# Optimization experiments

Measured on AMD Instinct MI355X. Metric: run time of the kernel, lower is better.

The kernel has to match this reference:

```python
import jax, jax.numpy as jnp
import numpy as np

N_NODES = 16384
N_EDGES = 98304
N_CAND = 1024
# GAT config from default __init__: heads=[8,8,1], features=[3,64,128,64]
LAYERS = [
    (3, 8, 64, True, True),      # (f_in, n_heads, f_out, concat, elu)
    (512, 8, 128, True, True),
    (1024, 1, 64, False, False),
]


def _gat_layer(x, src, tgt, W, a_src, a_tgt, b, skipW, nh, fo, concat, act):
    n = x.shape[0]
    proj = (x @ W).reshape(n, nh, fo)                 # [N, NH, F]
    s_src = jnp.einsum('nhf,hf->nh', proj, a_src)     # [N, NH]
    s_tgt = jnp.einsum('nhf,hf->nh', proj, a_tgt)
    e = jax.nn.leaky_relu(s_src[src] + s_tgt[tgt], 0.2)   # [E, NH]
    # numerically stable segment softmax over incoming edges of each target node
    e_max = jax.ops.segment_max(e, tgt, num_segments=n)
    ex = jnp.exp(e - jax.lax.stop_gradient(e_max)[tgt])
    denom = jax.ops.segment_sum(ex, tgt, num_segments=n)
    alpha = ex / (denom[tgt] + 1e-16)                 # [E, NH]
    agg = jax.ops.segment_sum(proj[src] * alpha[:, :, None], tgt, num_segments=n)
    out = agg + (x @ skipW).reshape(n, nh, fo)        # skip connection (projected)
    out = out.reshape(n, nh * fo) if concat else out.mean(axis=1)
    out = out + b
    return jax.nn.elu(out) if act else out


def setup_inputs() -> dict:
    key = jax.random.key(0)
    ks = iter(jax.random.split(key, 32))
    d = {}
    d['fea'] = jax.random.normal(next(ks), (N_NODES, 3), dtype=jnp.float32)
    d['edge_index'] = jax.random.randint(next(ks), (2, N_EDGES), 0, N_NODES, dtype=jnp.int32)
    d['candidates_id'] = jax.random.randint(next(ks), (N_CAND,), 0, N_NODES, dtype=jnp.int32)
    for i, (fi, nh, fo, concat, _) in enumerate(LAYERS):
        sc = 1.0 / np.sqrt(fi)
        d[f'W{i}'] = jax.random.normal(next(ks), (fi, nh * fo), dtype=jnp.float32) * sc
        d[f'a_src{i}'] = jax.random.normal(next(ks), (nh, fo), dtype=jnp.float32) * 0.1
        d[f'a_tgt{i}'] = jax.random.normal(next(ks), (nh, fo), dtype=jnp.float32) * 0.1
        d[f'b{i}'] = jnp.zeros((nh * fo if concat else fo,), dtype=jnp.float32)
        d[f'skip{i}'] = jax.random.normal(next(ks), (fi, nh * fo), dtype=jnp.float32) * sc
    # MLP head build_mlp(256, 3, 64, 1): 64->256 Tanh 256->256 Tanh 256->1
    for j, (a, bdim) in enumerate([(64, 256), (256, 256), (256, 1)], start=1):
        d[f'mW{j}'] = jax.random.normal(next(ks), (a, bdim), dtype=jnp.float32) / np.sqrt(a)
        d[f'mb{j}'] = jnp.zeros((bdim,), dtype=jnp.float32)
    return d


def reference(fea, edge_index, candidates_id,
              W0, a_src0, a_tgt0, b0, skip0,
              W1, a_src1, a_tgt1, b1, skip1,
              W2, a_src2, a_tgt2, b2, skip2,
              mW1, mb1, mW2, mb2, mW3, mb3):
    src, tgt = edge_index[0], edge_index[1]
    x = fea
    params = [(W0, a_src0, a_tgt0, b0, skip0), (W1, a_src1, a_tgt1, b1, skip1),
              (W2, a_src2, a_tgt2, b2, skip2)]
    for (fi, nh, fo, concat, act), (W, asr, atg, b, sk) in zip(LAYERS, params):
        x = _gat_layer(x, src, tgt, W, asr, atg, b, sk, nh, fo, concat, act)
    cand = x[candidates_id]                              # [C, 64]
    h = jnp.tanh(cand @ mW1 + mb1)
    h = jnp.tanh(h @ mW2 + mb2)
    prob = (h @ mW3 + mb3).squeeze(-1)                   # [C]
    return prob, candidates_id
```

## Files before the change

### kernel.cpp

```cpp
#include <hip/hip_runtime.h>
#include <cmath>

#define N_NODES 16384
#define N_EDGES 98304
#define N_CAND  1024

typedef __bf16 bf16x8 __attribute__((ext_vector_type(8)));
typedef short  s16x8  __attribute__((ext_vector_type(8)));
typedef float  f32x4  __attribute__((ext_vector_type(4)));
typedef unsigned short u16x2 __attribute__((ext_vector_type(2)));
typedef unsigned short u16x4 __attribute__((ext_vector_type(4)));

__device__ __forceinline__ unsigned short f2bf(float x) {
    unsigned u = __float_as_uint(x);
    return (unsigned short)((u + 0x7fffu + ((u >> 16) & 1u)) >> 16);
}
__device__ __forceinline__ float bf2f(unsigned short b) {
    return __uint_as_float((unsigned)b << 16);
}

#define GLL(gp, lp) __builtin_amdgcn_global_load_lds(                          \
    (const __attribute__((address_space(1))) unsigned int*)(const void*)(gp),  \
    (__attribute__((address_space(3))) unsigned int*)(void*)(lp), 16, 0, 0)

__global__ __launch_bounds__(256) void k_hist(const int* __restrict__ tgt,
                                              int* __restrict__ deg) {
    int e = blockIdx.x * 256 + threadIdx.x;
    if (e < N_EDGES) atomicAdd(&deg[tgt[e]], 1);
}

__global__ __launch_bounds__(256) void k_scan_all(const int* __restrict__ deg,
                                                  int* __restrict__ off,
                                                  int* __restrict__ cursor) {
    __shared__ int ts[256];
    int tid = threadIdx.x;
    const int4* d4 = (const int4*)(deg + tid * 64);
    int s = 0;
    #pragma unroll
    for (int i = 0; i < 16; ++i) {
        int4 v = d4[i];
        s += v.x + v.y + v.z + v.w;
    }
    ts[tid] = s;
    __syncthreads();
    for (int o = 1; o < 256; o <<= 1) {
        int t = (tid >= o) ? ts[tid - o] : 0;
        __syncthreads();
        ts[tid] += t;
        __syncthreads();
    }
    int run = ts[tid] - s;
    int4* o4 = (int4*)(off + tid * 64);
    int4* c4 = (int4*)(cursor + tid * 64);
    #pragma unroll
    for (int i = 0; i < 16; ++i) {
        int4 v = d4[i];
        int4 ov;
        ov.x = run; run += v.x;
        ov.y = run; run += v.y;
        ov.z = run; run += v.z;
        ov.w = run; run += v.w;
        o4[i] = ov;
        c4[i] = ov;
    }
    if (tid == 255) off[N_NODES] = run;
}

__global__ __launch_bounds__(256) void k_scatter(const int* __restrict__ ei,
                                                 int* __restrict__ cursor,
                                                 int* __restrict__ csrc) {
    int e = blockIdx.x * 256 + threadIdx.x;
    if (e < N_EDGES) {
        int s = ei[e];
        int t = ei[N_EDGES + e];
        int pos = atomicAdd(&cursor[t], 1);
        csrc[pos] = s;
    }
}

__global__ __launch_bounds__(256) void k_l0s(const float* __restrict__ fea,
                                             const float* __restrict__ W0,
                                             const float* __restrict__ as,
                                             const float* __restrict__ at,
                                             float* __restrict__ ssrc,
                                             float* __restrict__ stgt) {
    int n = blockIdx.x, tid = threadIdx.x;
    float f0 = fea[n * 3 + 0], f1 = fea[n * 3 + 1], f2 = fea[n * 3 + 2];
    int c1 = tid, c2 = tid + 256;
    float p1 = f0 * W0[c1] + f1 * W0[512 + c1] + f2 * W0[1024 + c1];
    float p2 = f0 * W0[c2] + f1 * W0[512 + c2] + f2 * W0[1024 + c2];
    float vs1 = p1 * as[c1], vt1 = p1 * at[c1];
    float vs2 = p2 * as[c2], vt2 = p2 * at[c2];
    #pragma unroll
    for (int o = 32; o; o >>= 1) {
        vs1 += __shfl_xor(vs1, o); vt1 += __shfl_xor(vt1, o);
        vs2 += __shfl_xor(vs2, o); vt2 += __shfl_xor(vt2, o);
    }
    int lane = tid & 63, w = tid >> 6;
    if (lane == 0) {
        ssrc[n * 8 + w]     = vs1;  stgt[n * 8 + w]     = vt1;
        ssrc[n * 8 + w + 4] = vs2;  stgt[n * 8 + w + 4] = vt2;
    }
}

__device__ __forceinline__ void pack_slot(const float* __restrict__ src0,
                                          const float* __restrict__ src1,
                                          int splitN, int NTOT, int NKB, int s,
                                          unsigned short* __restrict__ hi,
                                          unsigned short* __restrict__ lo) {
    int nb = s / (NKB * 512);
    int rem = s - nb * (NKB * 512);
    int kb = rem >> 9;
    int sl = rem & 511;
    int c = sl >> 7, n = sl & 127;
    int col = nb * 128 + n;
    const float* src;
    int cc, stride;
    if (col < splitN) { src = src0; cc = col; stride = splitN; }
    else              { src = src1; cc = col - splitN; stride = NTOT - splitN; }
    int k0 = kb * 32 + c * 8;
    s16x8 hv, lv;
    #pragma unroll
    for (int j = 0; j < 8; ++j) {
        float w = src[(size_t)(k0 + j) * stride + cc];
        unsigned short h = f2bf(w);
        hv[j] = (short)h;
        lv[j] = (short)f2bf(w - bf2f(h));
    }
    *(s16x8*)(hi + (size_t)s * 8) = hv;
    *(s16x8*)(lo + (size_t)s * 8) = lv;
}

__global__ __launch_bounds__(256) void k_pack_all(
    const float* __restrict__ W1, const float* __restrict__ sk1,
    unsigned short* __restrict__ pw1h, unsigned short* __restrict__ pw1l,
    const float* __restrict__ W2, const float* __restrict__ sk2,
    unsigned short* __restrict__ pw2h, unsigned short* __restrict__ pw2l) {
    int s = blockIdx.x * 256 + threadIdx.x;
    if (s < 131072) {
        pack_slot(W1, sk1, 1024, 2048, 16, s, pw1h, pw1l);
    } else {
        int s2 = s - 131072;
        if (s2 < 16384) pack_slot(W2, sk2, 64, 128, 32, s2, pw2h, pw2l);
    }
}

template <int F, int NTOT, int KS>
__global__ __launch_bounds__(256, 2) void k_gemm_mfma(
    const unsigned short* __restrict__ Xhi, const unsigned short* __restrict__ Xlo,
    const unsigned short* __restrict__ Wph, const unsigned short* __restrict__ Wpl,
    float* __restrict__ out0, float* __restrict__ out1, int splitN) {
    constexpr int NKB = F / 32;
    static_assert(KS == 1 || NTOT == 128, "split-K assumes single col-block");
    __shared__ unsigned short lds[2 * 16384];
    const int tid = threadIdx.x;
    const int bm  = blockIdx.y * 128;
    const int nb  = blockIdx.x;

    const int sA0 = tid, sA1 = tid + 256;
    const int rA0 = sA0 >> 2, rA1 = sA1 >> 2;
    const int cA0 = (sA0 & 3) ^ ((rA0 >> 1) & 3);
    const int cA1 = (sA1 & 3) ^ ((rA1 >> 1) & 3);
    const unsigned short* gAh0 = Xhi + (size_t)(bm + rA0) * F + cA0 * 8;
    const unsigned short* gAh1 = Xhi + (size_t)(bm + rA1) * F + cA1 * 8;
    const unsigned short* gAl0 = Xlo + (size_t)(bm + rA0) * F + cA0 * 8;
    const unsigned short* gAl1 = Xlo + (size_t)(bm + rA1) * F + cA1 * 8;
    const unsigned short* gBh  = Wph + (KS == 1 ? (size_t)nb * NKB * 4096 : 0);
    const unsigned short* gBl  = Wpl + (KS == 1 ? (size_t)nb * NKB * 4096 : 0);

    const int wave = tid >> 6, lane = tid & 63;
    const int wm = wave >> 1, wn = wave & 1;
    const int l15 = lane & 15, lc = lane >> 4;

    int offA[4], offB[4];
    #pragma unroll
    for (int mi = 0; mi < 4; ++mi) {
        int row = wm * 64 + mi * 16 + l15;
        int chp = lc ^ ((row >> 1) & 3);
        offA[mi] = row * 32 + chp * 8;
    }
    #pragma unroll
    for (int ni = 0; ni < 4; ++ni) {
        int n = wn * 64 + ni * 16 + l15;
        offB[ni] = 8192 + (lc * 128 + n) * 8;
    }

    f32x4 acc[4][4];
    #pragma unroll
    for (int i = 0; i < 4; ++i)
        #pragma unroll
        for (int j = 0; j < 4; ++j)
            acc[i][j] = (f32x4){0.f, 0.f, 0.f, 0.f};

    auto stage = [&](int kb, int buf) {
        unsigned short* l = &lds[buf * 16384];
        const size_t ka  = (size_t)kb * 32;
        const size_t kbb = (size_t)kb * 4096;
        GLL(gAh0 + ka, l + sA0 * 8);
        GLL(gAh1 + ka, l + sA1 * 8);
        GLL(gAl0 + ka, l + 4096 + sA0 * 8);
        GLL(gAl1 + ka, l + 4096 + sA1 * 8);
        GLL(gBh + kbb + sA0 * 8, l + 8192 + sA0 * 8);
        GLL(gBh + kbb + sA1 * 8, l + 8192 + sA1 * 8);
        GLL(gBl + kbb + sA0 * 8, l + 12288 + sA0 * 8);
        GLL(gBl + kbb + sA1 * 8, l + 12288 + sA1 * 8);
    };

    const int kb0 = (KS > 1) ? nb * (NKB / KS) : 0;
    const int kbN = (KS > 1) ? (NKB / KS) : NKB;

    stage(kb0, 0);
    __syncthreads();

    for (int ki = 0; ki < kbN; ++ki) {
        const int buf = ki & 1;
        if (ki + 1 < kbN) stage(kb0 + ki + 1, buf ^ 1);
        const unsigned short* l = &lds[buf * 16384];
        bf16x8 ah[4], al[4], bh[4], bl[4];
        #pragma unroll
        for (int mi = 0; mi < 4; ++mi) {
            ah[mi] = *(const bf16x8*)(l + offA[mi]);
            al[mi] = *(const bf16x8*)(l + 4096 + offA[mi]);
        }
        #pragma unroll
        for (int ni = 0; ni < 4; ++ni) {
            bh[ni] = *(const bf16x8*)(l + offB[ni]);
            bl[ni] = *(const bf16x8*)(l + 4096 + offB[ni]);
        }
        #pragma unroll
        for (int mi = 0; mi < 4; ++mi)
            #pragma unroll
            for (int ni = 0; ni < 4; ++ni) {
                acc[mi][ni] = __builtin_amdgcn_mfma_f32_16x16x32_bf16(ah[mi], bh[ni], acc[mi][ni], 0, 0, 0);
                acc[mi][ni] = __builtin_amdgcn_mfma_f32_16x16x32_bf16(ah[mi], bl[ni], acc[mi][ni], 0, 0, 0);
                acc[mi][ni] = __builtin_amdgcn_mfma_f32_16x16x32_bf16(al[mi], bh[ni], acc[mi][ni], 0, 0, 0);
            }
        __syncthreads();
    }

    if constexpr (KS > 1) {
        #pragma unroll
        for (int ni = 0; ni < 4; ++ni) {
            int col = wn * 64 + ni * 16 + l15;
            #pragma unroll
            for (int mi = 0; mi < 4; ++mi) {
                int row0 = bm + wm * 64 + mi * 16 + lc * 4;
                #pragma unroll
                for (int r = 0; r < 4; ++r)
                    out0[((size_t)nb * N_NODES + row0 + r) * NTOT + col] = acc[mi][ni][r];
            }
        }
    } else {
        #pragma unroll
        for (int ni = 0; ni < 4; ++ni) {
            int col = nb * 128 + wn * 64 + ni * 16 + l15;
            float* o;
            int cc, stride;
            if (col < splitN) { o = out0; cc = col; stride = splitN; }
            else              { o = out1; cc = col - splitN; stride = NTOT - splitN; }
            #pragma unroll
            for (int mi = 0; mi < 4; ++mi) {
                int row0 = bm + wm * 64 + mi * 16 + lc * 4;
                #pragma unroll
                for (int r = 0; r < 4; ++r)
                    o[(size_t)(row0 + r) * stride + cc] = acc[mi][ni][r];
            }
        }
    }
}

template <int H, int FO>
__global__ __launch_bounds__(256) void k_scores(const float* __restrict__ P,
                                                const float* __restrict__ asrc,
                                                const float* __restrict__ atgt,
                                                float* __restrict__ ssrc,
                                                float* __restrict__ stgt) {
    constexpr int K = H * FO;
    int gid  = blockIdx.x * 4 + (threadIdx.x >> 6);
    int lane = threadIdx.x & 63;
    int n = gid / H, h = gid - n * H;
    if (n >= N_NODES) return;
    float vs = 0.f, vt = 0.f;
    #pragma unroll
    for (int q = 0; q < FO / 64; ++q) {
        int f = lane + q * 64;
        float p = P[(size_t)n * K + h * FO + f];
        vs += p * asrc[h * FO + f];
        vt += p * atgt[h * FO + f];
    }
    #pragma unroll
    for (int o = 32; o; o >>= 1) {
        vs += __shfl_xor(vs, o);
        vt += __shfl_xor(vt, o);
    }
    if (lane == 0) {
        ssrc[n * H + h] = vs;
        stgt[n * H + h] = vt;
    }
}

__global__ __launch_bounds__(256) void k_red2s(const float* __restrict__ part,
                                               const float* __restrict__ as2,
                                               const float* __restrict__ at2,
                                               float* __restrict__ P2,
                                               float* __restrict__ S2,
                                               float* __restrict__ ssrc,
                                               float* __restrict__ stgt) {
    int tid = threadIdx.x;
    int node = blockIdx.x * 16 + (tid >> 4);
    int cg = tid & 15;
    int c0 = cg * 8;
    const float* p0 = part + (size_t)node * 128 + c0;
    float v[8];
    {
        float4 a = *(const float4*)(p0);
        float4 b = *(const float4*)(p0 + 4);
        v[0]=a.x; v[1]=a.y; v[2]=a.z; v[3]=a.w; v[4]=b.x; v[5]=b.y; v[6]=b.z; v[7]=b.w;
    }
    #pragma unroll
    for (int ks = 1; ks < 4; ++ks) {
        const float* pk = p0 + (size_t)ks * N_NODES * 128;
        float4 a = *(const float4*)(pk);
        float4 b = *(const float4*)(pk + 4);
        v[0]+=a.x; v[1]+=a.y; v[2]+=a.z; v[3]+=a.w; v[4]+=b.x; v[5]+=b.y; v[6]+=b.z; v[7]+=b.w;
    }
    if (cg < 8) {
        float s = 0.f, t = 0.f;
        #pragma unroll
        for (int j = 0; j < 8; ++j) {
            s += v[j] * as2[c0 + j];
            t += v[j] * at2[c0 + j];
        }
        #pragma unroll
        for (int o = 1; o < 8; o <<= 1) { s += __shfl_xor(s, o); t += __shfl_xor(t, o); }
        float* d = P2 + (size_t)node * 64 + c0;
        *(float4*)(d)     = make_float4(v[0], v[1], v[2], v[3]);
        *(float4*)(d + 4) = make_float4(v[4], v[5], v[6], v[7]);
        if (cg == 0) { ssrc[node] = s; stgt[node] = t; }
    } else {
        float* d = S2 + (size_t)node * 64 + (c0 - 64);
        *(float4*)(d)     = make_float4(v[0], v[1], v[2], v[3]);
        *(float4*)(d + 4) = make_float4(v[4], v[5], v[6], v[7]);
    }
}

__global__ __launch_bounds__(256) void k_attn0(
    const float* __restrict__ fea, const float* __restrict__ W0,
    const float* __restrict__ sk0, const float* __restrict__ ssrc,
    const float* __restrict__ stgt, const int* __restrict__ off,
    const int* __restrict__ csrc, const float* __restrict__ bias,
    unsigned short* __restrict__ ohi, unsigned short* __restrict__ olo) {
    constexpr int H = 8, K = 512;
    int n = blockIdx.x, tid = threadIdx.x;
    __shared__ float st[H], mh[H], dh[H];
    __shared__ int   srcs[256];
    __shared__ float sfea[256][3];
    __shared__ float av[256 * H];
    const int c0 = tid * 2, h0 = tid >> 5;

    float w00 = W0[c0],        w01 = W0[c0 + 1];
    float w10 = W0[512 + c0],  w11 = W0[512 + c0 + 1];
    float w20 = W0[1024 + c0], w21 = W0[1024 + c0 + 1];

    int d0 = off[n], deg = off[n + 1] - d0;
    if (tid < H) st[tid] = stgt[n * H + tid];
    __syncthreads();

    float a0 = 0.f, a1 = 0.f;

    if (deg <= 256) {
        int cnt = deg;
        if (tid < cnt) srcs[tid] = csrc[d0 + tid];
        __syncthreads();
        for (int idx = tid; idx < cnt * 3; idx += 256)
            sfea[idx / 3][idx % 3] = fea[srcs[idx / 3] * 3 + idx % 3];
        for (int idx = tid; idx < cnt * H; idx += 256) {
            int e = idx >> 3, h = idx & 7;
            float v = ssrc[srcs[e] * H + h] + st[h];
            av[idx] = (v >= 0.f) ? v : 0.2f * v;
        }
        __syncthreads();
        if (tid < H) {
            float m = -INFINITY;
            for (int e = 0; e < cnt; ++e) m = fmaxf(m, av[e * H + tid]);
            float s = 0.f;
            for (int e = 0; e < cnt; ++e) s += expf(av[e * H + tid] - m);
            mh[tid] = m;
            dh[tid] = 1.f / (s + 1e-16f);
        }
        __syncthreads();
        for (int idx = tid; idx < cnt * H; idx += 256) {
            int h = idx & 7;
            av[idx] = expf(av[idx] - mh[h]) * dh[h];
        }
        __syncthreads();
        for (int e = 0; e < cnt; ++e) {
            float al = av[e * H + h0];
            float f0 = sfea[e][0], f1 = sfea[e][1], f2 = sfea[e][2];
            a0 += (f0 * w00 + f1 * w10 + f2 * w20) * al;
            a1 += (f0 * w01 + f1 * w11 + f2 * w21) * al;
        }
    } else {
        if (tid < H) { mh[tid] = -INFINITY; dh[tid] = 0.f; }
        __syncthreads();
        for (int base = 0; base < deg; base += 256) {
            int cnt = min(256, deg - base);
            if (tid < cnt) srcs[tid] = csrc[d0 + base + tid];
            __syncthreads();
            for (int idx = tid; idx < cnt * H; idx += 256) {
                int e = idx >> 3, h = idx & 7;
                float v = ssrc[srcs[e] * H + h] + st[h];
                av[idx] = (v >= 0.f) ? v : 0.2f * v;
            }
            __syncthreads();
            if (tid < H) {
                float m = mh[tid], d = dh[tid];
                float cm = -INFINITY;
                for (int e = 0; e < cnt; ++e) cm = fmaxf(cm, av[e * H + tid]);
                float nm = fmaxf(m, cm);
                float s = 0.f;
                for (int e = 0; e < cnt; ++e) s += expf(av[e * H + tid] - nm);
                d = ((m == -INFINITY) ? 0.f : d * expf(m - nm)) + s;
                mh[tid] = nm;
                dh[tid] = d;
            }
            __syncthreads();
        }
        if (tid < H) dh[tid] = 1.f / (dh[tid] + 1e-16f);
        __syncthreads();
        for (int base = 0; base < deg; base += 256) {
            int cnt = min(256, deg - base);
            if (tid < cnt) srcs[tid] = csrc[d0 + base + tid];
            __syncthreads();
            for (int idx = tid; idx < cnt * 3; idx += 256)
                sfea[idx / 3][idx % 3] = fea[srcs[idx / 3] * 3 + idx % 3];
            for (int idx = tid; idx < cnt * H; idx += 256) {
                int e = idx >> 3, h = idx & 7;
                float v = ssrc[srcs[e] * H + h] + st[h];
                v = (v >= 0.f) ? v : 0.2f * v;
                av[idx] = expf(v - mh[h]) * dh[h];
            }
            __syncthreads();
            for (int e = 0; e < cnt; ++e) {
                float al = av[e * H + h0];
                float f0 = sfea[e][0], f1 = sfea[e][1], f2 = sfea[e][2];
                a0 += (f0 * w00 + f1 * w10 + f2 * w20) * al;
                a1 += (f0 * w01 + f1 * w11 + f2 * w21) * al;
            }
            __syncthreads();
        }
    }

    float f0 = fea[n * 3], f1 = fea[n * 3 + 1], f2 = fea[n * 3 + 2];
    float r0 = a0 + f0 * sk0[c0]     + f1 * sk0[512 + c0]     + f2 * sk0[1024 + c0]     + bias[c0];
    float r1 = a1 + f0 * sk0[c0 + 1] + f1 * sk0[512 + c0 + 1] + f2 * sk0[1024 + c0 + 1] + bias[c0 + 1];
    r0 = (r0 > 0.f) ? r0 : expm1f(r0);
    r1 = (r1 > 0.f) ? r1 : expm1f(r1);
    u16x2 hv, lv;
    unsigned short hb0 = f2bf(r0); hv[0] = hb0; lv[0] = f2bf(r0 - bf2f(hb0));
    unsigned short hb1 = f2bf(r1); hv[1] = hb1; lv[1] = f2bf(r1 - bf2f(hb1));
    *(u16x2*)(ohi + (size_t)n * K + c0) = hv;
    *(u16x2*)(olo + (size_t)n * K + c0) = lv;
}

template <int H, int FO, bool ACT, bool SPLIT, bool CAND>
__global__ __launch_bounds__(256) void k_attn_g(
    const float* __restrict__ P, const float* __restrict__ ssrc,
    const float* __restrict__ stgt, const int* __restrict__ off,
    const int* __restrict__ csrc, const float* __restrict__ bias,
    const float* __restrict__ skipin, float* __restrict__ outf,
    unsigned short* __restrict__ ohi, unsigned short* __restrict__ olo,
    const int* __restrict__ nidx) {
    constexpr int K   = H * FO;
    constexpr int VEC = (K / 256 >= 4) ? 4 : ((K / 256 >= 1) ? (K / 256) : 1);
    constexpr int NT  = K / VEC;
    int n = CAND ? nidx[blockIdx.x] : blockIdx.x;
    int orow = CAND ? blockIdx.x : n;
    int tid = threadIdx.x;
    __shared__ float st[H], mh[H], dh[H];
    __shared__ int   srcs[256];
    __shared__ float av[256 * H];

    const int c0 = (tid < NT ? tid : 0) * VEC;
    const int h0 = c0 / FO;
    const float* pc = P + c0;

    int d0 = off[n], deg = off[n + 1] - d0;
    if (tid < H) st[tid] = stgt[n * H + tid];
    __syncthreads();

    float acc[VEC];
    #pragma unroll
    for (int j = 0; j < VEC; ++j) acc[j] = 0.f;

    if (deg <= 256) {
        int cnt = deg;
        if (tid < cnt) srcs[tid] = csrc[d0 + tid];
        __syncthreads();
        for (int idx = tid; idx < cnt * H; idx += 256) {
            int e = idx / H, h = idx - (idx / H) * H;
            float v = ssrc[srcs[e] * H + h] + st[h];
            av[idx] = (v >= 0.f) ? v : 0.2f * v;
        }
        __syncthreads();
        if (tid < H) {
            float m = -INFINITY;
            for (int e = 0; e < cnt; ++e) m = fmaxf(m, av[e * H + tid]);
            float s = 0.f;
            for (int e = 0; e < cnt; ++e) s += expf(av[e * H + tid] - m);
            mh[tid] = m;
            dh[tid] = 1.f / (s + 1e-16f);
        }
        __syncthreads();
        for (int idx = tid; idx < cnt * H; idx += 256) {
            int h = idx - (idx / H) * H;
            av[idx] = expf(av[idx] - mh[h]) * dh[h];
        }
        __syncthreads();
        if (NT == 256 || tid < NT) {
            for (int e = 0; e < cnt; ++e) {
                float a = av[e * H + h0];
                if constexpr (VEC == 4) {
                    const float4 v = *(const float4*)(pc + (size_t)srcs[e] * K);
                    acc[0] += v.x * a; acc[1] += v.y * a;
                    acc[2] += v.z * a; acc[3] += v.w * a;
                } else {
                    acc[0] += pc[(size_t)srcs[e] * K] * a;
                }
            }
        }
    } else {
        if (tid < H) { mh[tid] = -INFINITY; dh[tid] = 0.f; }
        __syncthreads();
        for (int base = 0; base < deg; base += 256) {
            int cnt = min(256, deg - base);
            if (tid < cnt) srcs[tid] = csrc[d0 + base + tid];
            __syncthreads();
            for (int idx = tid; idx < cnt * H; idx += 256) {
                int e = idx / H, h = idx - (idx / H) * H;
                float v = ssrc[srcs[e] * H + h] + st[h];
                av[idx] = (v >= 0.f) ? v : 0.2f * v;
            }
            __syncthreads();
            if (tid < H) {
                float m = mh[tid], d = dh[tid];
                float cm = -INFINITY;
                for (int e = 0; e < cnt; ++e) cm = fmaxf(cm, av[e * H + tid]);
                float nm = fmaxf(m, cm);
                float s = 0.f;
                for (int e = 0; e < cnt; ++e) s += expf(av[e * H + tid] - nm);
                d = ((m == -INFINITY) ? 0.f : d * expf(m - nm)) + s;
                mh[tid] = nm;
                dh[tid] = d;
            }
            __syncthreads();
        }
        if (tid < H) dh[tid] = 1.f / (dh[tid] + 1e-16f);
        __syncthreads();
        for (int base = 0; base < deg; base += 256) {
            int cnt = min(256, deg - base);
            if (tid < cnt) srcs[tid] = csrc[d0 + base + tid];
            __syncthreads();
            for (int idx = tid; idx < cnt * H; idx += 256) {
                int e = idx / H, h = idx - (idx / H) * H;
                float v = ssrc[srcs[e] * H + h] + st[h];
                v = (v >= 0.f) ? v : 0.2f * v;
                av[idx] = expf(v - mh[h]) * dh[h];
            }
            __syncthreads();
            if (NT == 256 || tid < NT) {
                for (int e = 0; e < cnt; ++e) {
                    float a = av[e * H + h0];
                    if constexpr (VEC == 4) {
                        const float4 v = *(const float4*)(pc + (size_t)srcs[e] * K);
                        acc[0] += v.x * a; acc[1] += v.y * a;
                        acc[2] += v.z * a; acc[3] += v.w * a;
                    } else {
                        acc[0] += pc[(size_t)srcs[e] * K] * a;
                    }
                }
            }
            __syncthreads();
        }
    }

    if (NT == 256 || tid < NT) {
        float r[VEC];
        if constexpr (VEC == 4) {
            const float4 s4 = *(const float4*)(skipin + (size_t)n * K + c0);
            r[0] = acc[0] + s4.x; r[1] = acc[1] + s4.y;
            r[2] = acc[2] + s4.z; r[3] = acc[3] + s4.w;
        } else {
            r[0] = acc[0] + skipin[(size_t)n * K + c0];
        }
        #pragma unroll
        for (int j = 0; j < VEC; ++j) {
            r[j] += bias[c0 + j];
            if (ACT) r[j] = (r[j] > 0.f) ? r[j] : expm1f(r[j]);
        }
        if constexpr (SPLIT) {
            if constexpr (VEC == 4) {
                u16x4 hv, lv;
                #pragma unroll
                for (int j = 0; j < 4; ++j) {
                    unsigned short hb = f2bf(r[j]);
                    hv[j] = hb; lv[j] = f2bf(r[j] - bf2f(hb));
                }
                *(u16x4*)(ohi + (size_t)orow * K + c0) = hv;
                *(u16x4*)(olo + (size_t)orow * K + c0) = lv;
            } else {
                unsigned short hb = f2bf(r[0]);
                ohi[(size_t)orow * K + c0] = hb;
                olo[(size_t)orow * K + c0] = f2bf(r[0] - bf2f(hb));
            }
        } else {
            if constexpr (VEC == 4) {
                *(float4*)(outf + (size_t)orow * K + c0) =
                    make_float4(r[0], r[1], r[2], r[3]);
            } else {
                outf[(size_t)orow * K + c0] = r[0];
            }
        }
    }
}

__global__ __launch_bounds__(256) void k_mlp(const float* __restrict__ X3c,
                                             const int* __restrict__ cid,
                                             const float* __restrict__ W1,
                                             const float* __restrict__ b1,
                                             const float* __restrict__ W2,
                                             const float* __restrict__ b2,
                                             const float* __restrict__ W3,
                                             const float* __restrict__ b3,
                                             float* __restrict__ out) {
    __shared__ float cf[16][64];
    __shared__ float h1s[16][256];
    __shared__ float red[16][4];
    int tid = threadIdx.x;
    int cbase = blockIdx.x * 16;
    for (int i = tid; i < 16 * 64; i += 256)
        cf[i >> 6][i & 63] = X3c[(size_t)cbase * 64 + i];
    __syncthreads();
    float a[16];
    #pragma unroll
    for (int ci = 0; ci < 16; ++ci) a[ci] = b1[tid];
    for (int k = 0; k < 64; ++k) {
        float wv = W1[k * 256 + tid];
        #pragma unroll
        for (int ci = 0; ci < 16; ++ci) a[ci] += cf[ci][k] * wv;
    }
    #pragma unroll
    for (int ci = 0; ci < 16; ++ci) h1s[ci][tid] = tanhf(a[ci]);
    __syncthreads();
    #pragma unroll
    for (int ci = 0; ci < 16; ++ci) a[ci] = b2[tid];
    for (int k = 0; k < 256; ++k) {
        float wv = W2[k * 256 + tid];
        #pragma unroll
        for (int ci = 0; ci < 16; ++ci) a[ci] += h1s[ci][k] * wv;
    }
    float w3 = W3[tid];
    int lane = tid & 63, wv_ = tid >> 6;
    #pragma unroll
    for (int ci = 0; ci < 16; ++ci) {
        float v = tanhf(a[ci]) * w3;
        #pragma unroll
        for (int o = 32; o; o >>= 1) v += __shfl_xor(v, o);
        if (lane == 0) red[ci][wv_] = v;
    }
    __syncthreads();
    if (tid < 16) {
        int c = cbase + tid;
        out[c] = red[tid][0] + red[tid][1] + red[tid][2] + red[tid][3] + b3[0];
        out[N_CAND + c] = (float)cid[c];
    }
}

extern "C" void kernel_launch(void* const* d_in, const int* in_sizes, int n_in,
                              void* d_out, int out_size, void* d_ws, size_t ws_size,
                              hipStream_t stream) {
    const float* fea  = (const float*)d_in[0];
    const int*   ei   = (const int*)d_in[1];
    const int*   cid  = (const int*)d_in[2];
    const float* W0   = (const float*)d_in[3];
    const float* as0  = (const float*)d_in[4];
    const float* at0  = (const float*)d_in[5];
    const float* b0   = (const float*)d_in[6];
    const float* sk0  = (const float*)d_in[7];
    const float* W1   = (const float*)d_in[8];
    const float* as1  = (const float*)d_in[9];
    const float* at1  = (const float*)d_in[10];
    const float* b1   = (const float*)d_in[11];
    const float* sk1  = (const float*)d_in[12];
    const float* W2   = (const float*)d_in[13];
    const float* as2  = (const float*)d_in[14];
    const float* at2  = (const float*)d_in[15];
    const float* b2   = (const float*)d_in[16];
    const float* sk2  = (const float*)d_in[17];
    const float* mW1  = (const float*)d_in[18];
    const float* mb1  = (const float*)d_in[19];
    const float* mW2  = (const float*)d_in[20];
    const float* mb2  = (const float*)d_in[21];
    const float* mW3  = (const float*)d_in[22];
    const float* mb3  = (const float*)d_in[23];

    char* w = (char*)d_ws;
    auto alloc = [&](size_t bytes) -> void* {
        void* p = (void*)w;
        w += (bytes + 255) & ~(size_t)255;
        return p;
    };
    int*   deg    = (int*)alloc((size_t)N_NODES * 4);
    int*   off    = (int*)alloc((size_t)(N_NODES + 1) * 4);
    int*   cursor = (int*)alloc((size_t)N_NODES * 4);
    int*   csrc   = (int*)alloc((size_t)N_EDGES * 4);
    float* ssrc   = (float*)alloc((size_t)N_NODES * 8 * 4);
    float* stgt   = (float*)alloc((size_t)N_NODES * 8 * 4);
    float* P      = (float*)alloc((size_t)N_NODES * 1024 * 4);
    float* S      = (float*)alloc((size_t)N_NODES * 1024 * 4);
    unsigned short* Xs = (unsigned short*)alloc((size_t)N_NODES * 1024 * 4);
    unsigned short* pw1h = (unsigned short*)alloc((size_t)512 * 2048 * 2);
    unsigned short* pw1l = (unsigned short*)alloc((size_t)512 * 2048 * 2);
    unsigned short* pw2h = (unsigned short*)alloc((size_t)1024 * 128 * 2);
    unsigned short* pw2l = (unsigned short*)alloc((size_t)1024 * 128 * 2);

    unsigned short* X1hi = Xs;
    unsigned short* X1lo = Xs + (size_t)N_NODES * 512;
    unsigned short* X2hi = Xs;
    unsigned short* X2lo = Xs + (size_t)N_NODES * 1024;
    float* part = P;
    float* P2   = S;
    float* S2   = S + (size_t)N_NODES * 64;
    float* X3c  = S + (size_t)2 * N_NODES * 64;

    hipMemsetAsync(deg, 0, (size_t)N_NODES * 4, stream);
    k_hist<<<N_EDGES / 256, 256, 0, stream>>>(ei + N_EDGES, deg);
    k_scan_all<<<1, 256, 0, stream>>>(deg, off, cursor);
    k_scatter<<<N_EDGES / 256, 256, 0, stream>>>(ei, cursor, csrc);

    k_pack_all<<<576, 256, 0, stream>>>(W1, sk1, pw1h, pw1l, W2, sk2, pw2h, pw2l);

    k_l0s<<<N_NODES, 256, 0, stream>>>(fea, W0, as0, at0, ssrc, stgt);
    k_attn0<<<N_NODES, 256, 0, stream>>>(fea, W0, sk0, ssrc, stgt, off, csrc,
                                         b0, X1hi, X1lo);

    {
        dim3 g(16, N_NODES / 128);
        k_gemm_mfma<512, 2048, 1><<<g, 256, 0, stream>>>(
            X1hi, X1lo, pw1h, pw1l, P, S, 1024);
    }
    k_scores<8, 128><<<N_NODES * 8 / 4, 256, 0, stream>>>(P, as1, at1, ssrc, stgt);
    k_attn_g<8, 128, true, true, false><<<N_NODES, 256, 0, stream>>>(
        P, ssrc, stgt, off, csrc, b1, S, nullptr, X2hi, X2lo, nullptr);

    {
        dim3 g(4, N_NODES / 128);
        k_gemm_mfma<1024, 128, 4><<<g, 256, 0, stream>>>(
            X2hi, X2lo, pw2h, pw2l, part, nullptr, 128);
    }
    k_red2s<<<N_NODES / 16, 256, 0, stream>>>(part, as2, at2, P2, S2, ssrc, stgt);
    k_attn_g<1, 64, false, false, true><<<N_CAND, 256, 0, stream>>>(
        P2, ssrc, stgt, off, csrc, b2, S2, X3c, nullptr, nullptr, cid);

    k_mlp<<<N_CAND / 16, 256, 0, stream>>>(X3c, cid, mW1, mb1, mW2, mb2, mW3, mb3,
                                           (float*)d_out);
}
```

Baseline: 477.8 us.

## Map one wavefront per node in attention kernels with shuffle-based online softmax

```diff
diff --git a/kernel.cpp b/kernel.cpp
--- a/kernel.cpp
+++ b/kernel.cpp
@@ -8,8 +8,8 @@
 typedef __bf16 bf16x8 __attribute__((ext_vector_type(8)));
 typedef short  s16x8  __attribute__((ext_vector_type(8)));
 typedef float  f32x4  __attribute__((ext_vector_type(4)));
-typedef unsigned short u16x2 __attribute__((ext_vector_type(2)));
 typedef unsigned short u16x4 __attribute__((ext_vector_type(4)));
+typedef unsigned short u16x8 __attribute__((ext_vector_type(8)));
 
 __device__ __forceinline__ unsigned short f2bf(float x) {
     unsigned u = __float_as_uint(x);
@@ -344,127 +344,87 @@
     }
 }
 
-__global__ __launch_bounds__(256) void k_attn0(
+__global__ __launch_bounds__(256) void k_attn0_w(
     const float* __restrict__ fea, const float* __restrict__ W0,
     const float* __restrict__ sk0, const float* __restrict__ ssrc,
     const float* __restrict__ stgt, const int* __restrict__ off,
     const int* __restrict__ csrc, const float* __restrict__ bias,
     unsigned short* __restrict__ ohi, unsigned short* __restrict__ olo) {
-    constexpr int H = 8, K = 512;
-    int n = blockIdx.x, tid = threadIdx.x;
-    __shared__ float st[H], mh[H], dh[H];
-    __shared__ int   srcs[256];
-    __shared__ float sfea[256][3];
-    __shared__ float av[256 * H];
-    const int c0 = tid * 2, h0 = tid >> 5;
-
-    float w00 = W0[c0],        w01 = W0[c0 + 1];
-    float w10 = W0[512 + c0],  w11 = W0[512 + c0 + 1];
-    float w20 = W0[1024 + c0], w21 = W0[1024 + c0 + 1];
-
+    constexpr int H = 8, K = 512, EPC = 8;
+    int wv = threadIdx.x >> 6, lane = threadIdx.x & 63;
+    int n = blockIdx.x * 4 + wv;
+    int he = lane >> 3, hh = lane & 7;
+    int c0 = lane * 8;
+
+    float w0r[8], w1r[8], w2r[8];
+    #pragma unroll
+    for (int j = 0; j < 8; ++j) {
+        w0r[j] = W0[c0 + j];
+        w1r[j] = W0[512 + c0 + j];
+        w2r[j] = W0[1024 + c0 + j];
+    }
+    float st_h = stgt[n * H + hh];
     int d0 = off[n], deg = off[n + 1] - d0;
-    if (tid < H) st[tid] = stgt[n * H + tid];
-    __syncthreads();
-
-    float a0 = 0.f, a1 = 0.f;
-
-    if (deg <= 256) {
-        int cnt = deg;
-        if (tid < cnt) srcs[tid] = csrc[d0 + tid];
-        __syncthreads();
-        for (int idx = tid; idx < cnt * 3; idx += 256)
-            sfea[idx / 3][idx % 3] = fea[srcs[idx / 3] * 3 + idx % 3];
-        for (int idx = tid; idx < cnt * H; idx += 256) {
-            int e = idx >> 3, h = idx & 7;
-            float v = ssrc[srcs[e] * H + h] + st[h];
-            av[idx] = (v >= 0.f) ? v : 0.2f * v;
-        }
-        __syncthreads();
-        if (tid < H) {
-            float m = -INFINITY;
-            for (int e = 0; e < cnt; ++e) m = fmaxf(m, av[e * H + tid]);
-            float s = 0.f;
-            for (int e = 0; e < cnt; ++e) s += expf(av[e * H + tid] - m);
-            mh[tid] = m;
-            dh[tid] = 1.f / (s + 1e-16f);
-        }
-        __syncthreads();
-        for (int idx = tid; idx < cnt * H; idx += 256) {
-            int h = idx & 7;
-            av[idx] = expf(av[idx] - mh[h]) * dh[h];
-        }
-        __syncthreads();
+
+    float m = -INFINITY, d = 0.f;
+    for (int base = 0; base < deg; base += EPC) {
+        int cnt = min(EPC, deg - base);
+        float s = -INFINITY;
+        if (he < cnt) {
+            int se = csrc[d0 + base + he];
+            float v = ssrc[se * H + hh] + st_h;
+            s = (v >= 0.f) ? v : 0.2f * v;
+        }
+        float cm = s;
+        #pragma unroll
+        for (int o = H; o < 64; o <<= 1) cm = fmaxf(cm, __shfl_xor(cm, o));
+        float nm = fmaxf(m, cm);
+        float pe = (he < cnt) ? expf(s - nm) : 0.f;
+        #pragma unroll
+        for (int o = H; o < 64; o <<= 1) pe += __shfl_xor(pe, o);
+        d = ((m == -INFINITY) ? 0.f : d * expf(m - nm)) + pe;
+        m = nm;
+    }
+    float dinv = 1.f / (d + 1e-16f);
+
+    float acc[8] = {0.f, 0.f, 0.f, 0.f, 0.f, 0.f, 0.f, 0.f};
+    for (int base = 0; base < deg; base += EPC) {
+        int cnt = min(EPC, deg - base);
+        int msrc = 0;
+        float al = 0.f;
+        if (he < cnt) {
+            msrc = csrc[d0 + base + he];
+            float v = ssrc[msrc * H + hh] + st_h;
+            v = (v >= 0.f) ? v : 0.2f * v;
+            al = expf(v - m) * dinv;
+        }
         for (int e = 0; e < cnt; ++e) {
-            float al = av[e * H + h0];
-            float f0 = sfea[e][0], f1 = sfea[e][1], f2 = sfea[e][2];
-            a0 += (f0 * w00 + f1 * w10 + f2 * w20) * al;
-            a1 += (f0 * w01 + f1 * w11 + f2 * w21) * al;
-        }
-    } else {
-        if (tid < H) { mh[tid] = -INFINITY; dh[tid] = 0.f; }
-        __syncthreads();
-        for (int base = 0; base < deg; base += 256) {
-            int cnt = min(256, deg - base);
-            if (tid < cnt) srcs[tid] = csrc[d0 + base + tid];
-            __syncthreads();
-            for (int idx = tid; idx < cnt * H; idx += 256) {
-                int e = idx >> 3, h = idx & 7;
-                float v = ssrc[srcs[e] * H + h] + st[h];
-                av[idx] = (v >= 0.f) ? v : 0.2f * v;
-            }
-            __syncthreads();
-            if (tid < H) {
-                float m = mh[tid], d = dh[tid];
-                float cm = -INFINITY;
-                for (int e = 0; e < cnt; ++e) cm = fmaxf(cm, av[e * H + tid]);
-                float nm = fmaxf(m, cm);
-                float s = 0.f;
-                for (int e = 0; e < cnt; ++e) s += expf(av[e * H + tid] - nm);
-                d = ((m == -INFINITY) ? 0.f : d * expf(m - nm)) + s;
-                mh[tid] = nm;
-                dh[tid] = d;
-            }
-            __syncthreads();
-        }
-        if (tid < H) dh[tid] = 1.f / (dh[tid] + 1e-16f);
-        __syncthreads();
-        for (int base = 0; base < deg; base += 256) {
-            int cnt = min(256, deg - base);
-            if (tid < cnt) srcs[tid] = csrc[d0 + base + tid];
-            __syncthreads();
-            for (int idx = tid; idx < cnt * 3; idx += 256)
-                sfea[idx / 3][idx % 3] = fea[srcs[idx / 3] * 3 + idx % 3];
-            for (int idx = tid; idx < cnt * H; idx += 256) {
-                int e = idx >> 3, h = idx & 7;
-                float v = ssrc[srcs[e] * H + h] + st[h];
-                v = (v >= 0.f) ? v : 0.2f * v;
-                av[idx] = expf(v - mh[h]) * dh[h];
-            }
-            __syncthreads();
-            for (int e = 0; e < cnt; ++e) {
-                float al = av[e * H + h0];
-                float f0 = sfea[e][0], f1 = sfea[e][1], f2 = sfea[e][2];
-                a0 += (f0 * w00 + f1 * w10 + f2 * w20) * al;
-                a1 += (f0 * w01 + f1 * w11 + f2 * w21) * al;
-            }
-            __syncthreads();
+            int se = __shfl(msrc, e * 8);
+            float f0 = fea[se * 3], f1 = fea[se * 3 + 1], f2 = fea[se * 3 + 2];
+            float a = __shfl(al, e * 8 + (lane >> 3));
+            #pragma unroll
+            for (int j = 0; j < 8; ++j)
+                acc[j] += (f0 * w0r[j] + f1 * w1r[j] + f2 * w2r[j]) * a;
         }
     }
 
     float f0 = fea[n * 3], f1 = fea[n * 3 + 1], f2 = fea[n * 3 + 2];
-    float r0 = a0 + f0 * sk0[c0]     + f1 * sk0[512 + c0]     + f2 * sk0[1024 + c0]     + bias[c0];
-    float r1 = a1 + f0 * sk0[c0 + 1] + f1 * sk0[512 + c0 + 1] + f2 * sk0[1024 + c0 + 1] + bias[c0 + 1];
-    r0 = (r0 > 0.f) ? r0 : expm1f(r0);
-    r1 = (r1 > 0.f) ? r1 : expm1f(r1);
-    u16x2 hv, lv;
-    unsigned short hb0 = f2bf(r0); hv[0] = hb0; lv[0] = f2bf(r0 - bf2f(hb0));
-    unsigned short hb1 = f2bf(r1); hv[1] = hb1; lv[1] = f2bf(r1 - bf2f(hb1));
-    *(u16x2*)(ohi + (size_t)n * K + c0) = hv;
-    *(u16x2*)(olo + (size_t)n * K + c0) = lv;
+    u16x8 hv, lv;
+    #pragma unroll
+    for (int j = 0; j < 8; ++j) {
+        float r = acc[j] + f0 * sk0[c0 + j] + f1 * sk0[512 + c0 + j]
+                + f2 * sk0[1024 + c0 + j] + bias[c0 + j];
+        r = (r > 0.f) ? r : expm1f(r);
+        unsigned short hb = f2bf(r);
+        hv[j] = hb;
+        lv[j] = f2bf(r - bf2f(hb));
+    }
+    *(u16x8*)(ohi + (size_t)n * K + c0) = hv;
+    *(u16x8*)(olo + (size_t)n * K + c0) = lv;
 }
 
 template <int H, int FO, bool ACT, bool SPLIT, bool CAND>
-__global__ __launch_bounds__(256) void k_attn_g(
+__global__ __launch_bounds__(256) void k_attn_w(
     const float* __restrict__ P, const float* __restrict__ ssrc,
     const float* __restrict__ stgt, const int* __restrict__ off,
     const int* __restrict__ csrc, const float* __restrict__ bias,
@@ -472,153 +432,92 @@
     unsigned short* __restrict__ ohi, unsigned short* __restrict__ olo,
     const int* __restrict__ nidx) {
     constexpr int K   = H * FO;
-    constexpr int VEC = (K / 256 >= 4) ? 4 : ((K / 256 >= 1) ? (K / 256) : 1);
-    constexpr int NT  = K / VEC;
-    int n = CAND ? nidx[blockIdx.x] : blockIdx.x;
-    int orow = CAND ? blockIdx.x : n;
-    int tid = threadIdx.x;
-    __shared__ float st[H], mh[H], dh[H];
-    __shared__ int   srcs[256];
-    __shared__ float av[256 * H];
-
-    const int c0 = (tid < NT ? tid : 0) * VEC;
-    const int h0 = c0 / FO;
-    const float* pc = P + c0;
-
+    constexpr int EPC = 64 / H;
+    constexpr int NC  = (K + 255) / 256;
+    int wv = threadIdx.x >> 6, lane = threadIdx.x & 63;
+    int idx = blockIdx.x * 4 + wv;
+    int n = CAND ? nidx[idx] : idx;
+    int orow = CAND ? idx : n;
+    int he = lane / H, hh = lane % H;
+
+    float st_h = stgt[n * H + hh];
     int d0 = off[n], deg = off[n + 1] - d0;
-    if (tid < H) st[tid] = stgt[n * H + tid];
-    __syncthreads();
-
-    float acc[VEC];
-    #pragma unroll
-    for (int j = 0; j < VEC; ++j) acc[j] = 0.f;
-
-    if (deg <= 256) {
-        int cnt = deg;
-        if (tid < cnt) srcs[tid] = csrc[d0 + tid];
-        __syncthreads();
-        for (int idx = tid; idx < cnt * H; idx += 256) {
-            int e = idx / H, h = idx - (idx / H) * H;
-            float v = ssrc[srcs[e] * H + h] + st[h];
-            av[idx] = (v >= 0.f) ? v : 0.2f * v;
-        }
-        __syncthreads();
-        if (tid < H) {
-            float m = -INFINITY;
-            for (int e = 0; e < cnt; ++e) m = fmaxf(m, av[e * H + tid]);
-            float s = 0.f;
-            for (int e = 0; e < cnt; ++e) s += expf(av[e * H + tid] - m);
-            mh[tid] = m;
-            dh[tid] = 1.f / (s + 1e-16f);
-        }
-        __syncthreads();
-        for (int idx = tid; idx < cnt * H; idx += 256) {
-            int h = idx - (idx / H) * H;
-            av[idx] = expf(av[idx] - mh[h]) * dh[h];
-        }
-        __syncthreads();
-        if (NT == 256 || tid < NT) {
-            for (int e = 0; e < cnt; ++e) {
-                float a = av[e * H + h0];
-                if constexpr (VEC == 4) {
-                    const float4 v = *(const float4*)(pc + (size_t)srcs[e] * K);
-                    acc[0] += v.x * a; acc[1] += v.y * a;
-                    acc[2] += v.z * a; acc[3] += v.w * a;
-                } else {
-                    acc[0] += pc[(size_t)srcs[e] * K] * a;
+
+    float m = -INFINITY, d = 0.f;
+    for (int base = 0; base < deg; base += EPC) {
+        int cnt = min(EPC, deg - base);
+        float s = -INFINITY;
+        if (he < cnt) {
+            int se = csrc[d0 + base + he];
+            float v = ssrc[se * H + hh] + st_h;
+            s = (v >= 0.f) ? v : 0.2f * v;
+        }
+        float cm = s;
+        #pragma unroll
+        for (int o = H; o < 64; o <<= 1) cm = fmaxf(cm, __shfl_xor(cm, o));
+        float nm = fmaxf(m, cm);
+        float pe = (he < cnt) ? expf(s - nm) : 0.f;
+        #pragma unroll
+        for (int o = H; o < 64; o <<= 1) pe += __shfl_xor(pe, o);
+        d = ((m == -INFINITY) ? 0.f : d * expf(m - nm)) + pe;
+        m = nm;
+    }
+    float dinv = 1.f / (d + 1e-16f);
+
+    float4 acc[NC];
+    #pragma unroll
+    for (int c = 0; c < NC; ++c) acc[c] = make_float4(0.f, 0.f, 0.f, 0.f);
+
+    for (int base = 0; base < deg; base += EPC) {
+        int cnt = min(EPC, deg - base);
+        int msrc = 0;
+        float al = 0.f;
+        if (he < cnt) {
+            msrc = csrc[d0 + base + he];
+            float v = ssrc[msrc * H + hh] + st_h;
+            v = (v >= 0.f) ? v : 0.2f * v;
+            al = expf(v - m) * dinv;
+        }
+        for (int e = 0; e < cnt; ++e) {
+            int se = __shfl(msrc, e * H);
+            const float* pr = P + (size_t)se * K;
+            #pragma unroll
+            for (int c = 0; c < NC; ++c) {
+                int col = c * 256 + lane * 4;
+                if (K % 256 == 0 || col < K) {
+                    float a = __shfl(al, e * H + col / FO);
+                    float4 v = *(const float4*)(pr + col);
+                    acc[c].x += v.x * a; acc[c].y += v.y * a;
+                    acc[c].z += v.z * a; acc[c].w += v.w * a;
                 }
             }
         }
-    } else {
-        if (tid < H) { mh[tid] = -INFINITY; dh[tid] = 0.f; }
-        __syncthreads();
-        for (int base = 0; base < deg; base += 256) {
-            int cnt = min(256, deg - base);
-            if (tid < cnt) srcs[tid] = csrc[d0 + base + tid];
-            __syncthreads();
-            for (int idx = tid; idx < cnt * H; idx += 256) {
-                int e = idx / H, h = idx - (idx / H) * H;
-                float v = ssrc[srcs[e] * H + h] + st[h];
-                av[idx] = (v >= 0.f) ? v : 0.2f * v;
-            }
-            __syncthreads();
-            if (tid < H) {
-                float m = mh[tid], d = dh[tid];
-                float cm = -INFINITY;
-                for (int e = 0; e < cnt; ++e) cm = fmaxf(cm, av[e * H + tid]);
-                float nm = fmaxf(m, cm);
-                float s = 0.f;
-                for (int e = 0; e < cnt; ++e) s += expf(av[e * H + tid] - nm);
-                d = ((m == -INFINITY) ? 0.f : d * expf(m - nm)) + s;
-                mh[tid] = nm;
-                dh[tid] = d;
-            }
-            __syncthreads();
-        }
-        if (tid < H) dh[tid] = 1.f / (dh[tid] + 1e-16f);
-        __syncthreads();
-        for (int base = 0; base < deg; base += 256) {
-            int cnt = min(256, deg - base);
-            if (tid < cnt) srcs[tid] = csrc[d0 + base + tid];
-            __syncthreads();
-            for (int idx = tid; idx < cnt * H; idx += 256) {
-                int e = idx / H, h = idx - (idx / H) * H;
-                float v = ssrc[srcs[e] * H + h] + st[h];
-                v = (v >= 0.f) ? v : 0.2f * v;
-                av[idx] = expf(v - mh[h]) * dh[h];
-            }
-            __syncthreads();
-            if (NT == 256 || tid < NT) {
-                for (int e = 0; e < cnt; ++e) {
-                    float a = av[e * H + h0];
-                    if constexpr (VEC == 4) {
-                        const float4 v = *(const float4*)(pc + (size_t)srcs[e] * K);
-                        acc[0] += v.x * a; acc[1] += v.y * a;
-                        acc[2] += v.z * a; acc[3] += v.w * a;
-                    } else {
-                        acc[0] += pc[(size_t)srcs[e] * K] * a;
-                    }
-                }
-            }
-            __syncthreads();
-        }
-    }
-
-    if (NT == 256 || tid < NT) {
-        float r[VEC];
-        if constexpr (VEC == 4) {
-            const float4 s4 = *(const float4*)(skipin + (size_t)n * K + c0);
-            r[0] = acc[0] + s4.x; r[1] = acc[1] + s4.y;
-            r[2] = acc[2] + s4.z; r[3] = acc[3] + s4.w;
-        } else {
-            r[0] = acc[0] + skipin[(size_t)n * K + c0];
-        }
-        #pragma unroll
-        for (int j = 0; j < VEC; ++j) {
-            r[j] += bias[c0 + j];
-            if (ACT) r[j] = (r[j] > 0.f) ? r[j] : expm1f(r[j]);
-        }
-        if constexpr (SPLIT) {
-            if constexpr (VEC == 4) {
+    }
+
+    #pragma unroll
+    for (int c = 0; c < NC; ++c) {
+        int col = c * 256 + lane * 4;
+        if (K % 256 == 0 || col < K) {
+            const float4 s4 = *(const float4*)(skipin + (size_t)n * K + col);
+            const float4 b4 = *(const float4*)(bias + col);
+            float r[4] = {acc[c].x + s4.x + b4.x, acc[c].y + s4.y + b4.y,
+                          acc[c].z + s4.z + b4.z, acc[c].w + s4.w + b4.w};
+            #pragma unroll
+            for (int j = 0; j < 4; ++j)
+                if (ACT) r[j] = (r[j] > 0.f) ? r[j] : expm1f(r[j]);
+            if constexpr (SPLIT) {
                 u16x4 hv, lv;
                 #pragma unroll
                 for (int j = 0; j < 4; ++j) {
                     unsigned short hb = f2bf(r[j]);
-                    hv[j] = hb; lv[j] = f2bf(r[j] - bf2f(hb));
+                    hv[j] = hb;
+                    lv[j] = f2bf(r[j] - bf2f(hb));
                 }
-                *(u16x4*)(ohi + (size_t)orow * K + c0) = hv;
-                *(u16x4*)(olo + (size_t)orow * K + c0) = lv;
+                *(u16x4*)(ohi + (size_t)orow * K + col) = hv;
+                *(u16x4*)(olo + (size_t)orow * K + col) = lv;
             } else {
-                unsigned short hb = f2bf(r[0]);
-                ohi[(size_t)orow * K + c0] = hb;
-                olo[(size_t)orow * K + c0] = f2bf(r[0] - bf2f(hb));
-            }
-        } else {
-            if constexpr (VEC == 4) {
-                *(float4*)(outf + (size_t)orow * K + c0) =
+                *(float4*)(outf + (size_t)orow * K + col) =
                     make_float4(r[0], r[1], r[2], r[3]);
-            } else {
-                outf[(size_t)orow * K + c0] = r[0];
             }
         }
     }
@@ -741,8 +640,8 @@
     k_pack_all<<<576, 256, 0, stream>>>(W1, sk1, pw1h, pw1l, W2, sk2, pw2h, pw2l);
 
     k_l0s<<<N_NODES, 256, 0, stream>>>(fea, W0, as0, at0, ssrc, stgt);
-    k_attn0<<<N_NODES, 256, 0, stream>>>(fea, W0, sk0, ssrc, stgt, off, csrc,
-                                         b0, X1hi, X1lo);
+    k_attn0_w<<<N_NODES / 4, 256, 0, stream>>>(fea, W0, sk0, ssrc, stgt, off,
+                                               csrc, b0, X1hi, X1lo);
 
     {
         dim3 g(16, N_NODES / 128);
@@ -750,7 +649,7 @@
             X1hi, X1lo, pw1h, pw1l, P, S, 1024);
     }
     k_scores<8, 128><<<N_NODES * 8 / 4, 256, 0, stream>>>(P, as1, at1, ssrc, stgt);
-    k_attn_g<8, 128, true, true, false><<<N_NODES, 256, 0, stream>>>(
+    k_attn_w<8, 128, true, true, false><<<N_NODES / 4, 256, 0, stream>>>(
         P, ssrc, stgt, off, csrc, b1, S, nullptr, X2hi, X2lo, nullptr);
 
     {
@@ -759,7 +658,7 @@
             X2hi, X2lo, pw2h, pw2l, part, nullptr, 128);
     }
     k_red2s<<<N_NODES / 16, 256, 0, stream>>>(part, as2, at2, P2, S2, ssrc, stgt);
-    k_attn_g<1, 64, false, false, true><<<N_CAND, 256, 0, stream>>>(
+    k_attn_w<1, 64, false, false, true><<<N_CAND / 4, 256, 0, stream>>>(
         P2, ssrc, stgt, off, csrc, b2, S2, X3c, nullptr, nullptr, cid);
 
     k_mlp<<<N_CAND / 16, 256, 0, stream>>>(X3c, cid, mW1, mb1, mW2, mb2, mW3, mb3,
```

New measurement: 490.5 us. +2.7%, slower.
